# Performance work log

Hardware: AMD Instinct MI355X
Metric: run time of the kernel (lower is better)

Reference implementation:

```python
import jax, jax.numpy as jnp
import numpy as np

B, T, D = 2, 512, 512
NUM_SCALES, MIN_S, MAX_S = 10, 0.01, 1.0
SCALES_NP = np.logspace(np.log10(MIN_S), np.log10(MAX_S), NUM_SCALES)


def _golay():
    # extended Golay (24,12) generator exactly as in _initialize_golay_code
    G = np.zeros((12, 24), np.float32)
    for i in range(12):
        G[i, i] = 1.0
        for j in range(11):
            G[i, 12 + j] = (i + j) % 2
        G[i, 23] = G[i, :23].sum() % 2
    return jnp.asarray(G)

GOLAY = _golay()  # [12,24]


def setup_inputs() -> dict:
    key = jax.random.key(0)
    ks = jax.random.split(key, 6)
    return {
        'token_ids': jax.random.randint(ks[0], (B, T), 0, 1000000, dtype=jnp.int32),
        'resonances': jax.random.uniform(ks[1], (D,), minval=1.0, maxval=50.0, dtype=jnp.float32),
        'emb_scales': jnp.ones((D,), jnp.float32),
        'emb_shifts': jnp.zeros((D,), jnp.float32),
        'emb_norm': jnp.ones((1,), jnp.float32),
        'scale_weights': jnp.ones((NUM_SCALES,), jnp.float32),
        'fractal_bias': jnp.zeros((1,), jnp.float32),
        'frac_norm': jnp.ones((1,), jnp.float32),
        'W_enc': jax.random.normal(ks[2], (D, 24), jnp.float32) / np.float32(np.sqrt(D)),
        'b_enc': jnp.zeros((24,), jnp.float32),
        'W_dec': jax.random.normal(ks[3], (24, D), jnp.float32) / np.float32(np.sqrt(24)),
        'b_dec': jnp.zeros((D,), jnp.float32),
        'ecc_strength': jnp.full((1,), 0.1, jnp.float32),
        'energy_preservation': jnp.ones((1,), jnp.float32),
    }


def _fractal_dimension(signal, scale_weights, fractal_bias, frac_norm):
    # differentiable box-counting (GenuineFractalAnalyzer.compute_fractal_dimension)
    input_energy = jnp.linalg.norm(signal)
    s = signal.reshape(-1)  # [N]
    s = (s - s.min()) / (s.max() - s.min() + 1e-8)
    counts = []
    for scale_np in SCALES_NP:
        nb = int(round(1.0 / scale_np))  # static per scale: 100 ... 1
        edges = jnp.linspace(0.0, 1.0, nb + 1)
        lo, hi = edges[:-1][:, None], edges[1:][:, None]  # [nb,1]
        # vectorized over boxes instead of python loop over boxes
        in_box = jax.nn.sigmoid(10.0 * (s[None, :] - lo)) * jax.nn.sigmoid(10.0 * (hi - s[None, :]))  # [nb,N]
        occ = in_box.sum(axis=1)  # [nb]
        counts.append(jax.nn.sigmoid(occ - 0.5).sum())
    box_counts = jnp.stack(counts)  # [NUM_SCALES]
    weighted = box_counts * jax.nn.softmax(scale_weights)
    scales = jnp.asarray(SCALES_NP, jnp.float32)
    log_x = jnp.log(1.0 / scales)
    log_y = jnp.log(weighted + 1e-8)
    n = np.float32(NUM_SCALES)
    sx, sy = log_x.sum(), log_y.sum()
    sxy, sx2 = (log_x * log_y).sum(), (log_x ** 2).sum()
    slope = (n * sxy - sx * sy) / (n * sx2 - sx ** 2 + 1e-8)
    fd = jnp.clip(-slope + fractal_bias, 1.0, 2.5)  # [1]
    out_energy = jnp.linalg.norm(fd)
    return fd * frac_norm * input_energy / out_energy


def reference(token_ids, resonances, emb_scales, emb_shifts, emb_norm, scale_weights,
              fractal_bias, frac_norm, W_enc, b_enc, W_dec, b_dec, ecc_strength,
              energy_preservation):
    # --- GenuineEmbedding.batch_encode (vectorized over B,T,D) ---
    token_value = (token_ids % 1000000).astype(jnp.float32) / 1e6  # [B,T]
    pos = jnp.arange(T, dtype=jnp.float32)  # [T]
    angle = resonances[None, None, :] * (token_value[:, :, None] + pos[None, :, None])  # [B,T,D]
    c, sn = jnp.cos(angle), jnp.sin(angle)
    comp = c * (1.0 + sn) + sn * sn
    emb = comp * emb_scales + emb_shifts
    tok_norm = jnp.linalg.norm(emb, axis=-1, keepdims=True)
    emb = jnp.where(tok_norm > 0, emb * emb_norm / tok_norm, emb)

    # --- GenuineLeechLattice.encode_to_lattice ---
    ecc = ecc_strength[0]
    ep = energy_preservation[0]
    e_in = jnp.linalg.norm(emb, axis=-1, keepdims=True)  # b t 1
    proj = emb @ W_enc + b_enc  # [B,T,24]
    golay_enc = jnp.einsum('btl,kl->btk', proj, GOLAY)  # [B,T,12]
    latt = jnp.round(golay_enc / ecc) * ecc
    e_out = jnp.linalg.norm(latt, axis=-1, keepdims=True)
    latt = latt * (e_in / (e_out + 1e-8)) * ep

    # --- GenuineLeechLattice.decode_from_lattice ---
    e_in2 = jnp.linalg.norm(latt, axis=-1, keepdims=True)
    golay_dec = jnp.einsum('btk,kl->btl', latt, GOLAY)  # [B,T,24]
    corrected = jnp.where(jnp.abs(golay_dec) > ecc, golay_dec, 0.0)
    res = corrected @ W_dec + b_dec  # [B,T,D]
    e_out2 = jnp.linalg.norm(res, axis=-1, keepdims=True)
    res = res * (e_in2 / (e_out2 + 1e-8)) * ep

    # --- GenuineFractalAnalyzer on the corrected signal, then modulate ---
    fd = _fractal_dimension(res, scale_weights, fractal_bias, frac_norm)  # [1]
    return res * fd
```

## Files before the change

### kernel.cpp

```cpp
#include <hip/hip_runtime.h>
#include <math.h>

#define NT   1024
#define TT   512
#define DD   512


__device__ __forceinline__ float np_pairwise512(const float* x, int tid) {
    float r = 0.0f;
    if (tid < 32) {
        const int b = tid >> 3, j = tid & 7;
        const float* p = x + 128 * b + j;
        r = p[0];
        #pragma unroll
        for (int i = 1; i < 16; i++) r = __fadd_rn(r, p[8 * i]);
    }
    r = __fadd_rn(r, __shfl_down(r, 1, 64));
    r = __fadd_rn(r, __shfl_down(r, 2, 64));
    r = __fadd_rn(r, __shfl_down(r, 4, 64));
    r = __fadd_rn(r, __shfl_down(r, 8, 64));
    r = __fadd_rn(r, __shfl_down(r, 16, 64));
    return r;
}

__device__ __forceinline__ float np_pairwise12(const float* a) {
    float r = __fadd_rn(__fadd_rn(__fadd_rn(a[0], a[1]), __fadd_rn(a[2], a[3])),
                        __fadd_rn(__fadd_rn(a[4], a[5]), __fadd_rn(a[6], a[7])));
    r = __fadd_rn(r, a[8]);
    r = __fadd_rn(r, a[9]);
    r = __fadd_rn(r, a[10]);
    r = __fadd_rn(r, a[11]);
    return r;
}

__global__ __launch_bounds__(256) void token_kernel(
    const int*   __restrict__ token_ids,
    const float* __restrict__ resonances,
    const float* __restrict__ emb_scales,
    const float* __restrict__ emb_shifts,
    const float* __restrict__ emb_norm,
    const float* __restrict__ W_enc,
    const float* __restrict__ b_enc,
    const float* __restrict__ W_dec,
    const float* __restrict__ b_dec,
    const float* __restrict__ ecc_p,
    const float* __restrict__ ep_p,
    float*       __restrict__ out,
    double*      __restrict__ sumsq_acc)
{
    const int tok  = blockIdx.x;
    const int t    = tok % TT;
    const int tid  = threadIdx.x;
    const int lane = tid & 63;
    const int wave = tid >> 6;

    __shared__ float  sh_w[DD * 24];
    __shared__ float  sh_e[DD];
    __shared__ float  sh_x[DD];
    __shared__ float  sh_p[24];
    __shared__ float  sh_c[24];
    __shared__ float  sh_l[12];
    __shared__ float  sh_sc[4];
    __shared__ double sh_red[4];

    {
        const float4* src = (const float4*)W_enc;
        float4*       dst = (float4*)sh_w;
        #pragma unroll
        for (int i = 0; i < 12; i++)
            dst[tid + 256 * i] = src[tid + 256 * i];
    }

    const float ecc   = ecc_p[0];
    const float ep    = ep_p[0];
    const float enorm = emb_norm[0];

    const int   idv  = token_ids[tok];
    const float tv   = __fdiv_rn((float)idv, 1000000.0f);
    const float base = __fadd_rn(tv, (float)t);

    const int d0 = tid, d1 = tid + 256;
    float e0, e1;
    {
        const float a0 = __fmul_rn(resonances[d0], base);
        const float a1 = __fmul_rn(resonances[d1], base);
        double s0d, c0d, s1d, c1d;
        sincos((double)a0, &s0d, &c0d);
        sincos((double)a1, &s1d, &c1d);
        const float s0 = (float)s0d, c0 = (float)c0d;
        const float s1 = (float)s1d, c1 = (float)c1d;
        const float comp0 = __fadd_rn(__fmul_rn(c0, __fadd_rn(1.0f, s0)), __fmul_rn(s0, s0));
        const float comp1 = __fadd_rn(__fmul_rn(c1, __fadd_rn(1.0f, s1)), __fmul_rn(s1, s1));
        e0 = __fadd_rn(__fmul_rn(comp0, emb_scales[d0]), emb_shifts[d0]);
        e1 = __fadd_rn(__fmul_rn(comp1, emb_scales[d1]), emb_shifts[d1]);
    }
    sh_x[d0] = __fmul_rn(e0, e0);
    sh_x[d1] = __fmul_rn(e1, e1);
    __syncthreads();

    float ps = np_pairwise512(sh_x, tid);
    if (tid == 0) sh_sc[0] = __fsqrt_rn(ps);
    __syncthreads();
    const float tok_norm = sh_sc[0];
    if (tok_norm > 0.0f) {
        e0 = __fdiv_rn(__fmul_rn(e0, enorm), tok_norm);
        e1 = __fdiv_rn(__fmul_rn(e1, enorm), tok_norm);
    }
    sh_e[d0] = e0; sh_e[d1] = e1;
    sh_x[d0] = __fmul_rn(e0, e0);
    sh_x[d1] = __fmul_rn(e1, e1);
    __syncthreads();

    ps = np_pairwise512(sh_x, tid);
    const float e_in = __fsqrt_rn(ps);
    __syncthreads();

    if (tid < 24) {
        float acc = 0.0f;
        #pragma unroll 8
        for (int d = 0; d < DD; d++)
            acc = fmaf(sh_e[d], sh_w[d * 24 + tid], acc);
        sh_p[tid] = __fadd_rn(acc, b_enc[tid]);
    }
    __syncthreads();

    if (tid < 12) {
        const int k = tid;
        float g = sh_p[k];
        #pragma unroll
        for (int l = 12; l < 23; l++)
            if ((k + l) & 1) g = __fadd_rn(g, sh_p[l]);
        if (k & 1) g = __fadd_rn(g, sh_p[23]);
        sh_l[k] = __fmul_rn(rintf(__fdiv_rn(g, ecc)), ecc);
    }
    __syncthreads();

    if (tid == 0) {
        float sq[12];
        #pragma unroll
        for (int k = 0; k < 12; k++) sq[k] = __fmul_rn(sh_l[k], sh_l[k]);
        const float e_out = __fsqrt_rn(np_pairwise12(sq));
        const float m1 = __fdiv_rn(e_in, __fadd_rn(e_out, 1e-8f));
        #pragma unroll
        for (int k = 0; k < 12; k++) {
            const float lv = __fmul_rn(__fmul_rn(sh_l[k], m1), ep);
            sh_l[k] = lv;
            sq[k] = __fmul_rn(lv, lv);
        }
        sh_sc[2] = __fsqrt_rn(np_pairwise12(sq));
    }
    __syncthreads();

    if (tid < 24) {
        const int l = tid;
        float g;
        if (l < 12) {
            g = sh_l[l];
        } else if (l < 23) {
            g = 0.0f;
            #pragma unroll
            for (int k = 0; k < 12; k++)
                if ((k + l) & 1) g = __fadd_rn(g, sh_l[k]);
        } else {
            g = 0.0f;
            for (int k = 1; k < 12; k += 2) g = __fadd_rn(g, sh_l[k]);
        }
        sh_c[l] = (fabsf(g) > ecc) ? g : 0.0f;
    }
    __syncthreads();

    float r0 = 0.0f, r1 = 0.0f;
    #pragma unroll
    for (int l = 0; l < 24; l++) {
        const float cl = sh_c[l];
        r0 = fmaf(cl, W_dec[l * DD + d0], r0);
        r1 = fmaf(cl, W_dec[l * DD + d1], r1);
    }
    r0 = __fadd_rn(r0, b_dec[d0]);
    r1 = __fadd_rn(r1, b_dec[d1]);
    sh_x[d0] = __fmul_rn(r0, r0);
    sh_x[d1] = __fmul_rn(r1, r1);
    __syncthreads();
    ps = np_pairwise512(sh_x, tid);
    if (tid == 0) sh_sc[3] = __fsqrt_rn(ps);
    __syncthreads();

    const float m2 = __fdiv_rn(sh_sc[2], __fadd_rn(sh_sc[3], 1e-8f));
    const float f0 = __fmul_rn(__fmul_rn(r0, m2), ep);
    const float f1 = __fmul_rn(__fmul_rn(r1, m2), ep);
    out[tok * DD + d0] = f0;
    out[tok * DD + d1] = f1;

    double v4 = (double)f0 * (double)f0 + (double)f1 * (double)f1;
    for (int off = 32; off > 0; off >>= 1) v4 += __shfl_down(v4, off, 64);
    if (lane == 0) sh_red[wave] = v4;
    __syncthreads();
    if (tid == 0) atomicAdd(sumsq_acc, sh_red[0] + sh_red[1] + sh_red[2] + sh_red[3]);
}

__global__ __launch_bounds__(256) void scale_kernel(
    float* __restrict__ out,
    const double* __restrict__ sumsq,
    const float*  __restrict__ frac_norm)
{
    const int i = blockIdx.x * blockDim.x + threadIdx.x;
    const float factor = (float)((double)frac_norm[0] * sqrt(sumsq[0]));
    float4 r = ((const float4*)out)[i];
    r.x = __fmul_rn(r.x, factor);
    r.y = __fmul_rn(r.y, factor);
    r.z = __fmul_rn(r.z, factor);
    r.w = __fmul_rn(r.w, factor);
    ((float4*)out)[i] = r;
}

extern "C" void kernel_launch(void* const* d_in, const int* in_sizes, int n_in,
                              void* d_out, int out_size, void* d_ws, size_t ws_size,
                              hipStream_t stream)
{
    const int*   token_ids  = (const int*)  d_in[0];
    const float* resonances = (const float*)d_in[1];
    const float* emb_scales = (const float*)d_in[2];
    const float* emb_shifts = (const float*)d_in[3];
    const float* emb_norm   = (const float*)d_in[4];
    const float* frac_norm  = (const float*)d_in[7];
    const float* W_enc      = (const float*)d_in[8];
    const float* b_enc      = (const float*)d_in[9];
    const float* W_dec      = (const float*)d_in[10];
    const float* b_dec      = (const float*)d_in[11];
    const float* ecc        = (const float*)d_in[12];
    const float* ep         = (const float*)d_in[13];

    double* acc = (double*)d_ws;
    hipMemsetAsync(acc, 0, sizeof(double), stream);

    token_kernel<<<NT, 256, 0, stream>>>(token_ids, resonances, emb_scales, emb_shifts,
                                         emb_norm, W_enc, b_enc, W_dec, b_dec, ecc, ep,
                                         (float*)d_out, acc);
    scale_kernel<<<(NT * DD) / 1024, 256, 0, stream>>>((float*)d_out, acc, frac_norm);
}
```

Before: 111.7 us.

## Drop shared W_enc staging and replace atomic sum with partials reduce kernel

Removes the per-block copy of the full 48KB W_enc matrix into shared memory, so the 24-thread projection now reads W_enc straight from global/cache. This cuts LDS use from about 52KB per block, which should let more blocks reside per CU, and avoids a 48KB load per block. The global double atomicAdd and the memset are replaced by per-token partial sums written to workspace, a single-block reduce kernel that computes the scale factor, and a simpler scale kernel. The cost is an extra kernel launch and uncached-in-LDS strided global reads in the serial projection loop.

```diff
diff --git a/kernel.cpp b/kernel.cpp
--- a/kernel.cpp
+++ b/kernel.cpp
@@ -46,7 +46,7 @@
     const float* __restrict__ ecc_p,
     const float* __restrict__ ep_p,
     float*       __restrict__ out,
-    double*      __restrict__ sumsq_acc)
+    double*      __restrict__ partials)
 {
     const int tok  = blockIdx.x;
     const int t    = tok % TT;
@@ -54,7 +54,6 @@
     const int lane = tid & 63;
     const int wave = tid >> 6;
 
-    __shared__ float  sh_w[DD * 24];
     __shared__ float  sh_e[DD];
     __shared__ float  sh_x[DD];
     __shared__ float  sh_p[24];
@@ -62,14 +61,6 @@
     __shared__ float  sh_l[12];
     __shared__ float  sh_sc[4];
     __shared__ double sh_red[4];
-
-    {
-        const float4* src = (const float4*)W_enc;
-        float4*       dst = (float4*)sh_w;
-        #pragma unroll
-        for (int i = 0; i < 12; i++)
-            dst[tid + 256 * i] = src[tid + 256 * i];
-    }
 
     const float ecc   = ecc_p[0];
     const float ep    = ep_p[0];
@@ -119,7 +110,7 @@
         float acc = 0.0f;
         #pragma unroll 8
         for (int d = 0; d < DD; d++)
-            acc = fmaf(sh_e[d], sh_w[d * 24 + tid], acc);
+            acc = fmaf(sh_e[d], W_enc[d * 24 + tid], acc);
         sh_p[tid] = __fadd_rn(acc, b_enc[tid]);
     }
     __syncthreads();
@@ -195,16 +186,32 @@
     for (int off = 32; off > 0; off >>= 1) v4 += __shfl_down(v4, off, 64);
     if (lane == 0) sh_red[wave] = v4;
     __syncthreads();
-    if (tid == 0) atomicAdd(sumsq_acc, sh_red[0] + sh_red[1] + sh_red[2] + sh_red[3]);
+    if (tid == 0) partials[tok] = sh_red[0] + sh_red[1] + sh_red[2] + sh_red[3];
+}
+
+__global__ __launch_bounds__(256) void reduce_kernel(
+    const double* __restrict__ partials,
+    const float*  __restrict__ frac_norm,
+    float*        __restrict__ factor_out)
+{
+    const int tid = threadIdx.x;
+    __shared__ double sh[4];
+    double s = 0.0;
+    #pragma unroll
+    for (int i = 0; i < 4; i++) s += partials[tid + 256 * i];
+    for (int off = 32; off > 0; off >>= 1) s += __shfl_down(s, off, 64);
+    if ((tid & 63) == 0) sh[tid >> 6] = s;
+    __syncthreads();
+    if (tid == 0)
+        factor_out[0] = (float)((double)frac_norm[0] * sqrt(sh[0] + sh[1] + sh[2] + sh[3]));
 }
 
 __global__ __launch_bounds__(256) void scale_kernel(
     float* __restrict__ out,
-    const double* __restrict__ sumsq,
-    const float*  __restrict__ frac_norm)
+    const float* __restrict__ factor_p)
 {
     const int i = blockIdx.x * blockDim.x + threadIdx.x;
-    const float factor = (float)((double)frac_norm[0] * sqrt(sumsq[0]));
+    const float factor = factor_p[0];
     float4 r = ((const float4*)out)[i];
     r.x = __fmul_rn(r.x, factor);
     r.y = __fmul_rn(r.y, factor);
@@ -230,11 +237,12 @@
     const float* ecc        = (const float*)d_in[12];
     const float* ep         = (const float*)d_in[13];
 
-    double* acc = (double*)d_ws;
-    hipMemsetAsync(acc, 0, sizeof(double), stream);
+    double* partials = (double*)d_ws;
+    float*  factor   = (float*)((char*)d_ws + NT * sizeof(double));
 
     token_kernel<<<NT, 256, 0, stream>>>(token_ids, resonances, emb_scales, emb_shifts,
                                          emb_norm, W_enc, b_enc, W_dec, b_dec, ecc, ep,
-                                         (float*)d_out, acc);
-    scale_kernel<<<(NT * DD) / 1024, 256, 0, stream>>>((float*)d_out, acc, frac_norm);
-}
+                                         (float*)d_out, partials);
+    reduce_kernel<<<1, 256, 0, stream>>>(partials, frac_norm, factor);
+    scale_kernel<<<(NT * DD) / 1024, 256, 0, stream>>>((float*)d_out, factor);
+}
```

Result: faster. 105.9 us (-5.2%).
